# Kernel optimization log

Measured on AMD Instinct MI355X. Metric: run time of the kernel, lower is better.

## Reference

```python
import jax, jax.numpy as jnp
import numpy as np

N0, N1, N2, N3 = 200000, 50000, 12000, 3000
E0, E1, E2 = 500000, 120000, 30000
D_IN, D_H, D_OUT = 256, 256, 64


def setup_inputs() -> dict:
    key = jax.random.key(0)
    ks = jax.random.split(key, 16)
    s = 1.0 / np.sqrt(D_IN)
    return {
        "x": jax.random.normal(ks[0], (N0, D_IN), jnp.float32),
        "src0": jax.random.randint(ks[1], (E0,), 0, N0),
        "dst0": jax.random.randint(ks[2], (E0,), 0, N1),
        "src1": jax.random.randint(ks[3], (E1,), 0, N1),
        "dst1": jax.random.randint(ks[4], (E1,), 0, N2),
        "src2": jax.random.randint(ks[5], (E2,), 0, N2),
        "dst2": jax.random.randint(ks[6], (E2,), 0, N3),
        "num_dst0": N1, "num_dst1": N2, "num_dst2": N3,
        "Ws0": jax.random.normal(ks[7], (D_IN, D_H), jnp.float32) * s,
        "Wn0": jax.random.normal(ks[8], (D_IN, D_H), jnp.float32) * s,
        "b0": jnp.zeros((D_H,), jnp.float32),
        "Ws1": jax.random.normal(ks[9], (D_H, D_H), jnp.float32) * s,
        "Wn1": jax.random.normal(ks[10], (D_H, D_H), jnp.float32) * s,
        "b1": jnp.zeros((D_H,), jnp.float32),
        "Ws2": jax.random.normal(ks[11], (D_H, D_OUT), jnp.float32) * s,
        "Wn2": jax.random.normal(ks[12], (D_H, D_OUT), jnp.float32) * s,
        "b2": jnp.zeros((D_OUT,), jnp.float32),
    }


def sage_conv(src, dst, num_dst, h_src, Wn, Ws, b):
    # DGL SAGEConv(mean): fc_self(h_dst) + fc_neigh(mean_{in-edges} h_src) + bias
    h_dst = h_src[:num_dst]
    msg = h_src[src]                                          # [E, d] gather
    agg = jax.ops.segment_sum(msg, dst, num_segments=num_dst)  # [num_dst, d]
    deg = jax.ops.segment_sum(jnp.ones((dst.shape[0],), h_src.dtype), dst,
                              num_segments=num_dst)
    h_neigh = agg / jnp.maximum(deg, 1.0)[:, None]
    return h_dst @ Ws + h_neigh @ Wn + b


def reference(x, src0, dst0, src1, dst1, src2, dst2,
              num_dst0, num_dst1, num_dst2,
              Ws0, Wn0, b0, Ws1, Wn1, b1, Ws2, Wn2, b2):
    h = sage_conv(src0, dst0, num_dst0, x, Wn0, Ws0, b0)       # layer 0 (no act, per source)
    h = sage_conv(src1, dst1, num_dst1, h, Wn1, Ws1, b1)       # layer 1
    h = jax.nn.relu(h)                                         # activation after middle layer
    # dropout omitted (eval / deterministic mode)
    h = sage_conv(src2, dst2, num_dst2, h, Wn2, Ws2, b2)       # layer 2
    return h
```

## Files before the change

kernel.cpp:

```cpp
#include <hip/hip_runtime.h>

#define N0_SRC 200000
#define N1_DST 50000
#define N2_DST 12000
#define N3_DST 3000
#define NTOT_DST 65000
#define DH 256
#define DOUT 64
#define EMAX_TOT 650000

typedef __attribute__((ext_vector_type(8))) short short8;
typedef __attribute__((ext_vector_type(4))) float f32x4;

__device__ __forceinline__ ushort f2bf(float f) {
    union { float f; uint32_t u; } v; v.f = f;
    uint32_t r = (v.u + 0x7FFF + ((v.u >> 16) & 1)) >> 16;
    return (ushort)r;
}
__device__ __forceinline__ float bf2f(ushort u) {
    union { uint32_t u; float f; } v; v.u = ((uint32_t)u) << 16;
    return v.f;
}

__global__ void f32_to_bf16_kernel(const float* __restrict__ in,
                                   ushort* __restrict__ out, long n) {
    long i = ((long)blockIdx.x * 256 + threadIdx.x) * 4;
    if (i >= n) return;
    float4 v = *(const float4*)(in + i);
    ushort4 o;
    o.x = f2bf(v.x); o.y = f2bf(v.y); o.z = f2bf(v.z); o.w = f2bf(v.w);
    *(ushort4*)(out + i) = o;
}

__global__ void transpose_w_all(const float* __restrict__ W0, const float* __restrict__ W1,
                                const float* __restrict__ W2, const float* __restrict__ W3,
                                const float* __restrict__ W4, const float* __restrict__ W5,
                                ushort* __restrict__ out) {
    const float* W; int Ndim; ushort* o;
    switch (blockIdx.y) {
        case 0: W = W0; Ndim = 256; o = out; break;
        case 1: W = W1; Ndim = 256; o = out + 65536; break;
        case 2: W = W2; Ndim = 256; o = out + 131072; break;
        case 3: W = W3; Ndim = 256; o = out + 196608; break;
        case 4: W = W4; Ndim = 64;  o = out + 262144; break;
        default: W = W5; Ndim = 64; o = out + 278528; break;
    }
    int id = blockIdx.x * 256 + threadIdx.x;
    int n = id >> 8;
    int k = id & 255;
    if (n >= Ndim) return;
    o[id] = f2bf(W[k * Ndim + n]);
}

__global__ void hist3_kernel(const int* __restrict__ d0, int E0,
                             const int* __restrict__ d1, int E1,
                             const int* __restrict__ d2, int E2,
                             int* __restrict__ cnt) {
    int layer = blockIdx.y;
    const int* dst; int E; int base;
    if (layer == 0)      { dst = d0; E = E0; base = 0; }
    else if (layer == 1) { dst = d1; E = E1; base = N1_DST; }
    else                 { dst = d2; E = E2; base = N1_DST + N2_DST; }
    int e = blockIdx.x * 256 + threadIdx.x;
    if (e < E) atomicAdd(&cnt[base + dst[e]], 1);
}

__global__ void fill3_kernel(const int* __restrict__ s0, const int* __restrict__ d0, int E0,
                             const int* __restrict__ s1, const int* __restrict__ d1, int E1,
                             const int* __restrict__ s2, const int* __restrict__ d2, int E2,
                             int* __restrict__ cursor, int* __restrict__ eidx) {
    int layer = blockIdx.y;
    const int* src; const int* dst; int E; int base;
    if (layer == 0)      { src = s0; dst = d0; E = E0; base = 0; }
    else if (layer == 1) { src = s1; dst = d1; E = E1; base = N1_DST; }
    else                 { src = s2; dst = d2; E = E2; base = N1_DST + N2_DST; }
    int e = blockIdx.x * 256 + threadIdx.x;
    if (e < E) {
        int p = atomicAdd(&cursor[base + dst[e]], 1);
        eidx[p] = src[e];
    }
}

__global__ void scan_phase_a(const int* __restrict__ cnt, int* __restrict__ partial, int n) {
    __shared__ int red[4];
    int t = threadIdx.x;
    int i = blockIdx.x * 1024 + t * 4;
    int s = 0;
    if (i + 3 < n) {
        int4 v = *(const int4*)(cnt + i);
        s = v.x + v.y + v.z + v.w;
    }
#pragma unroll
    for (int d = 32; d; d >>= 1) s += __shfl_down(s, d, 64);
    if ((t & 63) == 0) red[t >> 6] = s;
    __syncthreads();
    if (t == 0) partial[blockIdx.x] = red[0] + red[1] + red[2] + red[3];
}

__global__ void scan_phase_b(int* __restrict__ partial, int nb) {
    int t = threadIdx.x;
    int own = (t < nb) ? partial[t] : 0;
    int v = own;
#pragma unroll
    for (int d = 1; d < 64; d <<= 1) {
        int u = __shfl_up(v, d, 64);
        if (t >= d) v += u;
    }
    if (t < nb) partial[t] = v - own;
}

__global__ void scan_phase_c(const int* __restrict__ cnt, const int* __restrict__ partial,
                             int* __restrict__ off, int* __restrict__ cursor, int n) {
    __shared__ int tsum[256];
    int t = threadIdx.x;
    int i = blockIdx.x * 1024 + t * 4;
    int4 c = make_int4(0, 0, 0, 0);
    if (i + 3 < n) c = *(const int4*)(cnt + i);
    int s = c.x + c.y + c.z + c.w;
    tsum[t] = s;
    __syncthreads();
#pragma unroll
    for (int d = 1; d < 256; d <<= 1) {
        int u = (t >= d) ? tsum[t - d] : 0;
        __syncthreads();
        tsum[t] += u;
        __syncthreads();
    }
    int base = partial[blockIdx.x] + tsum[t] - s;
    if (i + 3 < n) {
        int4 ov;
        ov.x = base;
        ov.y = ov.x + c.x;
        ov.z = ov.y + c.y;
        ov.w = ov.z + c.z;
        *(int4*)(off + i) = ov;
        *(int4*)(cursor + i) = ov;
        if (i + 4 == n) off[n] = ov.w + c.w;
    }
}

__global__ void gather_mean_bf16_kernel(const ushort* __restrict__ h,
                                        const int* __restrict__ off,
                                        const int* __restrict__ eidx,
                                        ushort* __restrict__ hn,
                                        int num_dst) {
    int w = blockIdx.x * 4 + (threadIdx.x >> 6);
    int lane = threadIdx.x & 63;
    if (w >= num_dst) return;
    int beg = off[w];
    int end = off[w + 1];
    float a0 = 0.f, a1 = 0.f, a2 = 0.f, a3 = 0.f;
    int i = beg;
    for (; i + 3 < end; i += 4) {
        int s0 = eidx[i], s1 = eidx[i + 1], s2 = eidx[i + 2], s3 = eidx[i + 3];
        ushort4 v0 = ((const ushort4*)(h + (size_t)s0 * DH))[lane];
        ushort4 v1 = ((const ushort4*)(h + (size_t)s1 * DH))[lane];
        ushort4 v2 = ((const ushort4*)(h + (size_t)s2 * DH))[lane];
        ushort4 v3 = ((const ushort4*)(h + (size_t)s3 * DH))[lane];
        a0 += (bf2f(v0.x) + bf2f(v1.x)) + (bf2f(v2.x) + bf2f(v3.x));
        a1 += (bf2f(v0.y) + bf2f(v1.y)) + (bf2f(v2.y) + bf2f(v3.y));
        a2 += (bf2f(v0.z) + bf2f(v1.z)) + (bf2f(v2.z) + bf2f(v3.z));
        a3 += (bf2f(v0.w) + bf2f(v1.w)) + (bf2f(v2.w) + bf2f(v3.w));
    }
    for (; i < end; ++i) {
        int s0 = eidx[i];
        ushort4 v0 = ((const ushort4*)(h + (size_t)s0 * DH))[lane];
        a0 += bf2f(v0.x); a1 += bf2f(v0.y); a2 += bf2f(v0.z); a3 += bf2f(v0.w);
    }
    float inv = 1.0f / fmaxf((float)(end - beg), 1.0f);
    ushort4 o;
    o.x = f2bf(a0 * inv); o.y = f2bf(a1 * inv);
    o.z = f2bf(a2 * inv); o.w = f2bf(a3 * inv);
    *(ushort4*)(hn + (size_t)w * DH + lane * 4) = o;
}

template <int BN, bool RELU, bool OUT_BF16>
__global__ void gemm_mfma(const ushort* __restrict__ Ad,
                          const ushort* __restrict__ An,
                          const ushort* __restrict__ Wst,
                          const ushort* __restrict__ Wnt,
                          const float* __restrict__ bias,
                          void* __restrict__ Cv,
                          int M, int N) {
    const int K = 256;
    const int LDK = 40;
    const int NT = BN / 16;
    __shared__ ushort As[128 * LDK];
    __shared__ ushort Bs[BN * LDK];

    int tid  = threadIdx.x;
    int lane = tid & 63;
    int wid  = tid >> 6;
    int quad = lane >> 4;
    int mr   = lane & 15;
    int row0 = blockIdx.y * 128;
    int col0 = blockIdx.x * BN;

    f32x4 acc[2][NT];
#pragma unroll
    for (int i = 0; i < 2; ++i)
#pragma unroll
        for (int j = 0; j < NT; ++j) acc[i][j] = (f32x4){0.f, 0.f, 0.f, 0.f};

    for (int pass = 0; pass < 2; ++pass) {
        const ushort* A  = pass ? An : Ad;
        const ushort* Wt = pass ? Wnt : Wst;
        for (int k0 = 0; k0 < K; k0 += 32) {
#pragma unroll
            for (int c = 0; c < 2; ++c) {
                int chunk = tid + c * 256;
                int r   = chunk >> 2;
                int seg = chunk & 3;
                int row = row0 + r;
                uint4 v = make_uint4(0u, 0u, 0u, 0u);
                if (row < M) v = *(const uint4*)(A + (size_t)row * K + k0 + seg * 8);
                *(uint4*)(&As[r * LDK + seg * 8]) = v;
            }
#pragma unroll
            for (int c = 0; c < BN / 64; ++c) {
                int chunk = tid + c * 256;
                int n   = chunk >> 2;
                int seg = chunk & 3;
                uint4 v = *(const uint4*)(Wt + (size_t)(col0 + n) * K + k0 + seg * 8);
                *(uint4*)(&Bs[n * LDK + seg * 8]) = v;
            }
            __syncthreads();
            short8 a[2], b[NT];
#pragma unroll
            for (int mt = 0; mt < 2; ++mt)
                a[mt] = *(const short8*)(&As[(wid * 32 + mt * 16 + mr) * LDK + quad * 8]);
#pragma unroll
            for (int nt = 0; nt < NT; ++nt)
                b[nt] = *(const short8*)(&Bs[(nt * 16 + mr) * LDK + quad * 8]);
#pragma unroll
            for (int mt = 0; mt < 2; ++mt)
#pragma unroll
                for (int nt = 0; nt < NT; ++nt)
                    acc[mt][nt] = __builtin_amdgcn_mfma_f32_16x16x32_bf16(
                        a[mt], b[nt], acc[mt][nt], 0, 0, 0);
            __syncthreads();
        }
    }

#pragma unroll
    for (int mt = 0; mt < 2; ++mt) {
#pragma unroll
        for (int i = 0; i < 4; ++i) {
            int row = row0 + wid * 32 + mt * 16 + quad * 4 + i;
            if (row >= M) continue;
#pragma unroll
            for (int nt = 0; nt < NT; ++nt) {
                int col = col0 + nt * 16 + mr;
                float v = acc[mt][nt][i] + bias[col];
                if (RELU) v = fmaxf(v, 0.0f);
                if (OUT_BF16) ((ushort*)Cv)[(size_t)row * N + col] = f2bf(v);
                else          ((float*)Cv)[(size_t)row * N + col] = v;
            }
        }
    }
}

extern "C" void kernel_launch(void* const* d_in, const int* in_sizes, int n_in,
                              void* d_out, int out_size, void* d_ws, size_t ws_size,
                              hipStream_t stream) {
    const float* x    = (const float*)d_in[0];
    const int* src0   = (const int*)d_in[1];
    const int* dst0   = (const int*)d_in[2];
    const int* src1   = (const int*)d_in[3];
    const int* dst1   = (const int*)d_in[4];
    const int* src2   = (const int*)d_in[5];
    const int* dst2   = (const int*)d_in[6];
    const float* Ws0  = (const float*)d_in[10];
    const float* Wn0  = (const float*)d_in[11];
    const float* b0   = (const float*)d_in[12];
    const float* Ws1  = (const float*)d_in[13];
    const float* Wn1  = (const float*)d_in[14];
    const float* b1   = (const float*)d_in[15];
    const float* Ws2  = (const float*)d_in[16];
    const float* Wn2  = (const float*)d_in[17];
    const float* b2   = (const float*)d_in[18];
    float* out = (float*)d_out;

    int E0 = in_sizes[1];
    int E1 = in_sizes[3];
    int E2 = in_sizes[5];

    ushort* wsu  = (ushort*)d_ws;
    ushort* xb   = wsu;
    ushort* hn0b = xb   + (size_t)N0_SRC * DH;
    ushort* h1b  = hn0b + (size_t)N1_DST * DH;
    ushort* hn1b = h1b  + (size_t)N1_DST * DH;
    ushort* h2b  = hn1b + (size_t)N2_DST * DH;
    ushort* hn2b = h2b  + (size_t)N2_DST * DH;
    ushort* Wt   = hn2b + (size_t)N3_DST * DH;
    ushort* Ws0t = Wt;
    ushort* Wn0t = Wt + 65536;
    ushort* Ws1t = Wt + 131072;
    ushort* Wn1t = Wt + 196608;
    ushort* Ws2t = Wt + 262144;
    ushort* Wn2t = Wt + 278528;
    int* cnt     = (int*)(Wt + 294912);
    int* off     = cnt + NTOT_DST;
    int* cursor  = off + NTOT_DST + 4;
    int* eidx    = cursor + NTOT_DST;
    int* partial = eidx + EMAX_TOT;

    long nxb = (long)N0_SRC * DH;
    f32_to_bf16_kernel<<<(int)((nxb / 4 + 255) / 256), 256, 0, stream>>>(x, xb, nxb);
    transpose_w_all<<<dim3(256, 6), 256, 0, stream>>>(Ws0, Wn0, Ws1, Wn1, Ws2, Wn2, Wt);

    int Emax = max(max(E0, E1), E2);
    int nb = (NTOT_DST + 1023) / 1024;
    hipMemsetAsync(cnt, 0, NTOT_DST * sizeof(int), stream);
    hist3_kernel<<<dim3((Emax + 255) / 256, 3), 256, 0, stream>>>(dst0, E0, dst1, E1, dst2, E2, cnt);
    scan_phase_a<<<nb, 256, 0, stream>>>(cnt, partial, NTOT_DST);
    scan_phase_b<<<1, 64, 0, stream>>>(partial, nb);
    scan_phase_c<<<nb, 256, 0, stream>>>(cnt, partial, off, cursor, NTOT_DST);
    fill3_kernel<<<dim3((Emax + 255) / 256, 3), 256, 0, stream>>>(
        src0, dst0, E0, src1, dst1, E1, src2, dst2, E2, cursor, eidx);

    const int* off0 = off;
    const int* off1 = off + N1_DST;
    const int* off2 = off + N1_DST + N2_DST;

    gather_mean_bf16_kernel<<<(N1_DST + 3) / 4, 256, 0, stream>>>(xb, off0, eidx, hn0b, N1_DST);
    {
        dim3 g(DH / 128, (N1_DST + 127) / 128);
        gemm_mfma<128, false, true><<<g, 256, 0, stream>>>(xb, hn0b, Ws0t, Wn0t, b0, h1b, N1_DST, DH);
    }

    gather_mean_bf16_kernel<<<(N2_DST + 3) / 4, 256, 0, stream>>>(h1b, off1, eidx, hn1b, N2_DST);
    {
        dim3 g(DH / 128, (N2_DST + 127) / 128);
        gemm_mfma<128, true, true><<<g, 256, 0, stream>>>(h1b, hn1b, Ws1t, Wn1t, b1, h2b, N2_DST, DH);
    }

    gather_mean_bf16_kernel<<<(N3_DST + 3) / 4, 256, 0, stream>>>(h2b, off2, eidx, hn2b, N3_DST);
    {
        dim3 g(DOUT / 64, (N3_DST + 127) / 128);
        gemm_mfma<64, false, false><<<g, 256, 0, stream>>>(h2b, hn2b, Ws2t, Wn2t, b2, out, N3_DST, DOUT);
    }
}
```

Before: 523.7 us.

## Rewrite dual GEMM with direct-to-LDS loads, swizzle, fused passes; fold memset

The GEMM is rebuilt to load the self and neighbor operands together in one K loop. Tiles go straight from global memory into LDS with global_load_lds and an XOR swizzle that replaces the padded layout, and each K step issues both MFMAs. The last layer uses a smaller 64-row tile to give more blocks, and the cnt memset is folded into the weight-transpose kernel to save a launch. The gather loop drops its scalar tail in favor of masked 4-wide loads, which does redundant loads on remainder edges.

After: 505.7 us. -3.4%, faster.

```diff
diff --git a/kernel.cpp b/kernel.cpp
--- a/kernel.cpp
+++ b/kernel.cpp
@@ -22,6 +22,13 @@
     return v.f;
 }
 
+__device__ __forceinline__ void gload16(const ushort* g, ushort* l) {
+    __builtin_amdgcn_global_load_lds(
+        (const __attribute__((address_space(1))) unsigned int*)g,
+        (__attribute__((address_space(3))) unsigned int*)l,
+        16, 0, 0);
+}
+
 __global__ void f32_to_bf16_kernel(const float* __restrict__ in,
                                    ushort* __restrict__ out, long n) {
     long i = ((long)blockIdx.x * 256 + threadIdx.x) * 4;
@@ -35,7 +42,11 @@
 __global__ void transpose_w_all(const float* __restrict__ W0, const float* __restrict__ W1,
                                 const float* __restrict__ W2, const float* __restrict__ W3,
                                 const float* __restrict__ W4, const float* __restrict__ W5,
-                                ushort* __restrict__ out) {
+                                ushort* __restrict__ out, int* __restrict__ cnt) {
+    if (blockIdx.y == 0) {
+        int z = blockIdx.x * 256 + threadIdx.x;
+        if (z < NTOT_DST) cnt[z] = 0;
+    }
     const float* W; int Ndim; ushort* o;
     switch (blockIdx.y) {
         case 0: W = W0; Ndim = 256; o = out; break;
@@ -150,22 +161,23 @@
     int beg = off[w];
     int end = off[w + 1];
     float a0 = 0.f, a1 = 0.f, a2 = 0.f, a3 = 0.f;
-    int i = beg;
-    for (; i + 3 < end; i += 4) {
-        int s0 = eidx[i], s1 = eidx[i + 1], s2 = eidx[i + 2], s3 = eidx[i + 3];
+    for (int i = beg; i < end; i += 4) {
+        int rem = end - i;
+        int j1 = i + (rem > 1 ? 1 : 0);
+        int j2 = i + (rem > 2 ? 2 : 0);
+        int j3 = i + (rem > 3 ? 3 : 0);
+        float m1 = rem > 1 ? 1.f : 0.f;
+        float m2 = rem > 2 ? 1.f : 0.f;
+        float m3 = rem > 3 ? 1.f : 0.f;
+        int s0 = eidx[i], s1 = eidx[j1], s2 = eidx[j2], s3 = eidx[j3];
         ushort4 v0 = ((const ushort4*)(h + (size_t)s0 * DH))[lane];
         ushort4 v1 = ((const ushort4*)(h + (size_t)s1 * DH))[lane];
         ushort4 v2 = ((const ushort4*)(h + (size_t)s2 * DH))[lane];
         ushort4 v3 = ((const ushort4*)(h + (size_t)s3 * DH))[lane];
-        a0 += (bf2f(v0.x) + bf2f(v1.x)) + (bf2f(v2.x) + bf2f(v3.x));
-        a1 += (bf2f(v0.y) + bf2f(v1.y)) + (bf2f(v2.y) + bf2f(v3.y));
-        a2 += (bf2f(v0.z) + bf2f(v1.z)) + (bf2f(v2.z) + bf2f(v3.z));
-        a3 += (bf2f(v0.w) + bf2f(v1.w)) + (bf2f(v2.w) + bf2f(v3.w));
-    }
-    for (; i < end; ++i) {
-        int s0 = eidx[i];
-        ushort4 v0 = ((const ushort4*)(h + (size_t)s0 * DH))[lane];
-        a0 += bf2f(v0.x); a1 += bf2f(v0.y); a2 += bf2f(v0.z); a3 += bf2f(v0.w);
+        a0 += bf2f(v0.x) + m1 * bf2f(v1.x) + m2 * bf2f(v2.x) + m3 * bf2f(v3.x);
+        a1 += bf2f(v0.y) + m1 * bf2f(v1.y) + m2 * bf2f(v2.y) + m3 * bf2f(v3.y);
+        a2 += bf2f(v0.z) + m1 * bf2f(v1.z) + m2 * bf2f(v2.z) + m3 * bf2f(v3.z);
+        a3 += bf2f(v0.w) + m1 * bf2f(v1.w) + m2 * bf2f(v2.w) + m3 * bf2f(v3.w);
     }
     float inv = 1.0f / fmaxf((float)(end - beg), 1.0f);
     ushort4 o;
@@ -174,79 +186,94 @@
     *(ushort4*)(hn + (size_t)w * DH + lane * 4) = o;
 }
 
-template <int BN, bool RELU, bool OUT_BF16>
-__global__ void gemm_mfma(const ushort* __restrict__ Ad,
-                          const ushort* __restrict__ An,
-                          const ushort* __restrict__ Wst,
-                          const ushort* __restrict__ Wnt,
-                          const float* __restrict__ bias,
-                          void* __restrict__ Cv,
-                          int M, int N) {
+template <int MT, int NT, bool RELU, bool OUT_BF16>
+__global__ __launch_bounds__(256) void gemm_dual(const ushort* __restrict__ Ad,
+                                                 const ushort* __restrict__ An,
+                                                 const ushort* __restrict__ Wst,
+                                                 const ushort* __restrict__ Wnt,
+                                                 const float* __restrict__ bias,
+                                                 void* __restrict__ Cv,
+                                                 int M, int N) {
     const int K = 256;
-    const int LDK = 40;
-    const int NT = BN / 16;
-    __shared__ ushort As[128 * LDK];
-    __shared__ ushort Bs[BN * LDK];
+    const int BM = MT * 64;
+    const int BN = NT * 16;
+    __shared__ __align__(16) ushort lds[(2 * BM + 2 * BN) * 32];
+    ushort* Asd = lds;
+    ushort* Asn = lds + BM * 32;
+    ushort* Bss = lds + 2 * BM * 32;
+    ushort* Bsn = lds + 2 * BM * 32 + BN * 32;
 
     int tid  = threadIdx.x;
     int lane = tid & 63;
     int wid  = tid >> 6;
-    int quad = lane >> 4;
+    int q    = lane >> 4;
     int mr   = lane & 15;
-    int row0 = blockIdx.y * 128;
+    int row0 = blockIdx.y * BM;
     int col0 = blockIdx.x * BN;
 
-    f32x4 acc[2][NT];
-#pragma unroll
-    for (int i = 0; i < 2; ++i)
+    f32x4 acc[MT][NT];
+#pragma unroll
+    for (int i = 0; i < MT; ++i)
 #pragma unroll
         for (int j = 0; j < NT; ++j) acc[i][j] = (f32x4){0.f, 0.f, 0.f, 0.f};
 
-    for (int pass = 0; pass < 2; ++pass) {
-        const ushort* A  = pass ? An : Ad;
-        const ushort* Wt = pass ? Wnt : Wst;
-        for (int k0 = 0; k0 < K; k0 += 32) {
-#pragma unroll
-            for (int c = 0; c < 2; ++c) {
-                int chunk = tid + c * 256;
-                int r   = chunk >> 2;
-                int seg = chunk & 3;
-                int row = row0 + r;
-                uint4 v = make_uint4(0u, 0u, 0u, 0u);
-                if (row < M) v = *(const uint4*)(A + (size_t)row * K + k0 + seg * 8);
-                *(uint4*)(&As[r * LDK + seg * 8]) = v;
+    for (int k0 = 0; k0 < K; k0 += 32) {
+#pragma unroll
+        for (int c = 0; c < MT; ++c) {
+            int chunk = c * 256 + tid;
+            int r   = chunk >> 2;
+            int sg  = (chunk & 3) ^ ((r >> 1) & 3);
+            int row = row0 + r;
+            if (row > M - 1) row = M - 1;
+            const ushort* gd = Ad + (size_t)row * K + k0 + sg * 8;
+            const ushort* gn = An + (size_t)row * K + k0 + sg * 8;
+            int cb = (c * 256 + (tid & ~63)) * 8;
+            gload16(gd, Asd + cb);
+            gload16(gn, Asn + cb);
+        }
+#pragma unroll
+        for (int c = 0; c < NT / 4; ++c) {
+            int chunk = c * 256 + tid;
+            int r  = chunk >> 2;
+            int sg = (chunk & 3) ^ ((r >> 1) & 3);
+            const ushort* gs = Wst + (size_t)(col0 + r) * K + k0 + sg * 8;
+            const ushort* gw = Wnt + (size_t)(col0 + r) * K + k0 + sg * 8;
+            int cb = (c * 256 + (tid & ~63)) * 8;
+            gload16(gs, Bss + cb);
+            gload16(gw, Bsn + cb);
+        }
+        __syncthreads();
+
+        short8 ad[MT], an[MT];
+#pragma unroll
+        for (int mt = 0; mt < MT; ++mt) {
+            int rho = wid * (MT * 16) + mt * 16 + mr;
+            int o   = rho * 32 + ((q ^ ((rho >> 1) & 3)) * 8);
+            ad[mt] = *(const short8*)(Asd + o);
+            an[mt] = *(const short8*)(Asn + o);
+        }
+#pragma unroll
+        for (int nt = 0; nt < NT; ++nt) {
+            int rho = nt * 16 + mr;
+            int o   = rho * 32 + ((q ^ ((rho >> 1) & 3)) * 8);
+            short8 bs = *(const short8*)(Bss + o);
+            short8 bn = *(const short8*)(Bsn + o);
+#pragma unroll
+            for (int mt = 0; mt < MT; ++mt) {
+                acc[mt][nt] = __builtin_amdgcn_mfma_f32_16x16x32_bf16(
+                    ad[mt], bs, acc[mt][nt], 0, 0, 0);
+                acc[mt][nt] = __builtin_amdgcn_mfma_f32_16x16x32_bf16(
+                    an[mt], bn, acc[mt][nt], 0, 0, 0);
             }
-#pragma unroll
-            for (int c = 0; c < BN / 64; ++c) {
-                int chunk = tid + c * 256;
-                int n   = chunk >> 2;
-                int seg = chunk & 3;
-                uint4 v = *(const uint4*)(Wt + (size_t)(col0 + n) * K + k0 + seg * 8);
-                *(uint4*)(&Bs[n * LDK + seg * 8]) = v;
-            }
-            __syncthreads();
-            short8 a[2], b[NT];
-#pragma unroll
-            for (int mt = 0; mt < 2; ++mt)
-                a[mt] = *(const short8*)(&As[(wid * 32 + mt * 16 + mr) * LDK + quad * 8]);
-#pragma unroll
-            for (int nt = 0; nt < NT; ++nt)
-                b[nt] = *(const short8*)(&Bs[(nt * 16 + mr) * LDK + quad * 8]);
-#pragma unroll
-            for (int mt = 0; mt < 2; ++mt)
-#pragma unroll
-                for (int nt = 0; nt < NT; ++nt)
-                    acc[mt][nt] = __builtin_amdgcn_mfma_f32_16x16x32_bf16(
-                        a[mt], b[nt], acc[mt][nt], 0, 0, 0);
-            __syncthreads();
-        }
-    }
-
-#pragma unroll
-    for (int mt = 0; mt < 2; ++mt) {
+        }
+        __syncthreads();
+    }
+
+#pragma unroll
+    for (int mt = 0; mt < MT; ++mt) {
 #pragma unroll
         for (int i = 0; i < 4; ++i) {
-            int row = row0 + wid * 32 + mt * 16 + quad * 4 + i;
+            int row = row0 + wid * (MT * 16) + mt * 16 + q * 4 + i;
             if (row >= M) continue;
 #pragma unroll
             for (int nt = 0; nt < NT; ++nt) {
@@ -307,11 +334,10 @@
 
     long nxb = (long)N0_SRC * DH;
     f32_to_bf16_kernel<<<(int)((nxb / 4 + 255) / 256), 256, 0, stream>>>(x, xb, nxb);
-    transpose_w_all<<<dim3(256, 6), 256, 0, stream>>>(Ws0, Wn0, Ws1, Wn1, Ws2, Wn2, Wt);
+    transpose_w_all<<<dim3(256, 6), 256, 0, stream>>>(Ws0, Wn0, Ws1, Wn1, Ws2, Wn2, Wt, cnt);
 
     int Emax = max(max(E0, E1), E2);
     int nb = (NTOT_DST + 1023) / 1024;
-    hipMemsetAsync(cnt, 0, NTOT_DST * sizeof(int), stream);
     hist3_kernel<<<dim3((Emax + 255) / 256, 3), 256, 0, stream>>>(dst0, E0, dst1, E1, dst2, E2, cnt);
     scan_phase_a<<<nb, 256, 0, stream>>>(cnt, partial, NTOT_DST);
     scan_phase_b<<<1, 64, 0, stream>>>(partial, nb);
@@ -324,20 +350,14 @@
     const int* off2 = off + N1_DST + N2_DST;
 
     gather_mean_bf16_kernel<<<(N1_DST + 3) / 4, 256, 0, stream>>>(xb, off0, eidx, hn0b, N1_DST);
-    {
-        dim3 g(DH / 128, (N1_DST + 127) / 128);
-        gemm_mfma<128, false, true><<<g, 256, 0, stream>>>(xb, hn0b, Ws0t, Wn0t, b0, h1b, N1_DST, DH);
-    }
+    gemm_dual<2, 8, false, true><<<dim3(DH / 128, (N1_DST + 127) / 128), 256, 0, stream>>>(
+        xb, hn0b, Ws0t, Wn0t, b0, h1b, N1_DST, DH);
 
     gather_mean_bf16_kernel<<<(N2_DST + 3) / 4, 256, 0, stream>>>(h1b, off1, eidx, hn1b, N2_DST);
-    {
-        dim3 g(DH / 128, (N2_DST + 127) / 128);
-        gemm_mfma<128, true, true><<<g, 256, 0, stream>>>(h1b, hn1b, Ws1t, Wn1t, b1, h2b, N2_DST, DH);
-    }
+    gemm_dual<2, 8, true, true><<<dim3(DH / 128, (N2_DST + 127) / 128), 256, 0, stream>>>(
+        h1b, hn1b, Ws1t, Wn1t, b1, h2b, N2_DST, DH);
 
     gather_mean_bf16_kernel<<<(N3_DST + 3) / 4, 256, 0, stream>>>(h2b, off2, eidx, hn2b, N3_DST);
-    {
-        dim3 g(DOUT / 64, (N3_DST + 127) / 128);
-        gemm_mfma<64, false, false><<<g, 256, 0, stream>>>(h2b, hn2b, Ws2t, Wn2t, b2, out, N3_DST, DOUT);
-    }
-}
+    gemm_dual<1, 4, false, false><<<dim3(DOUT / 64, (N3_DST + 63) / 64), 256, 0, stream>>>(
+        h2b, hn2b, Ws2t, Wn2t, b2, out, N3_DST, DOUT);
+}
```
